# Kernel optimization log

Measured on AMD Instinct MI355X. Metric: run time of the kernel, lower is better.

Reference implementation:

```python
import jax, jax.numpy as jnp
import numpy as np
import math

N_HEAD = 12
N_EMBD = 768

def setup_inputs() -> dict:
    key = jax.random.key(0)
    ks = jax.random.split(key, 5)
    B, T, C = 4, 2048, N_EMBD
    s_attn = 1.0 / math.sqrt(C)
    return {
        "x": jax.random.normal(ks[0], (B, T, C), jnp.float32),
        "w_attn": jax.random.normal(ks[1], (C, 3 * C), jnp.float32) * s_attn,
        "b_attn": jnp.zeros((3 * C,), jnp.float32),
        "w_proj": jax.random.normal(ks[2], (C, C), jnp.float32) * s_attn,
        "b_proj": jnp.zeros((C,), jnp.float32),
    }

def reference(x, w_attn, b_attn, w_proj, b_proj):
    B, T, C = x.shape
    H = N_HEAD
    D = C // H
    qkv = x @ w_attn + b_attn  # [B,T,3C]
    q, k, v = jnp.split(qkv, 3, axis=-1)
    # [B,T,C] -> [B,H,T,D]
    q = q.reshape(B, T, H, D).transpose(0, 2, 1, 3)
    k = k.reshape(B, T, H, D).transpose(0, 2, 1, 3)
    v = v.reshape(B, T, H, D).transpose(0, 2, 1, 3)
    att = jnp.einsum('bhqd,bhkd->bhqk', q, k) * (1.0 / math.sqrt(D))
    causal = jnp.tril(jnp.ones((T, T), bool))
    att = jnp.where(causal[None, None], att, -jnp.inf)
    att = jax.nn.softmax(att, axis=-1)
    y = jnp.einsum('bhqk,bhkd->bhqd', att, v)  # [B,H,T,D]
    y = y.transpose(0, 2, 1, 3).reshape(B, T, C)
    return y @ w_proj + b_proj
```

## Files before the change

### kernel.cpp

```cpp
#include <hip/hip_runtime.h>
#include <hip/hip_bf16.h>

typedef unsigned short u16;
typedef __attribute__((ext_vector_type(4))) short bf16x4;
typedef __attribute__((ext_vector_type(8))) short bf16x8;
typedef __attribute__((ext_vector_type(16))) float f32x16;

#define NB_ 4
#define NT_ 2048
#define NC_ 768
#define NH_ 12
#define ND_ 64
#define NM_ (NB_*NT_)
#define KC_ 24

#define SCQ_ 0.18033688011112042f

__device__ __forceinline__ u16 f2bf(float f){
  union { float f; unsigned u; } c; c.f = f;
  unsigned u = c.u;
  return (u16)((u + 0x7fffu + ((u>>16)&1u)) >> 16);
}

__device__ __forceinline__ unsigned pkbf(float a, float b){
  __hip_bfloat162 h = __float22bfloat162_rn(make_float2(a,b));
  union { __hip_bfloat162 h; unsigned u; } c; c.h = h; return c.u;
}

__device__ __forceinline__ f32x16 mfma32(bf16x8 a, bf16x8 b, f32x16 c){
  return __builtin_amdgcn_mfma_f32_32x32x16_bf16(a, b, c, 0, 0, 0);
}

__device__ __forceinline__ void gload_lds16(const void* g, void* l){
  __builtin_amdgcn_global_load_lds(
    (const __attribute__((address_space(1))) void*)g,
    (__attribute__((address_space(3))) void*)l, 16, 0, 0);
}


__global__ __launch_bounds__(256) void prep_k(
    const float* __restrict__ x, const float* __restrict__ wa,
    const float* __restrict__ wp, u16* __restrict__ xb,
    u16* __restrict__ wat, u16* __restrict__ wpt){
  __shared__ float tile[32][33];
  const int bid = blockIdx.x, t = threadIdx.x;
  if (bid < 6144){
    int i = bid*256 + t;
    float4 v = ((const float4*)x)[i];
    int row = i / (NC_/4), k4 = (i % (NC_/4))*4;
    size_t off = (((size_t)(row>>7)*KC_ + (k4>>5))*4 + ((k4>>3)&3))*1024 + (row&127)*8 + (k4&7);
    bf16x4 o;
    o[0]=(short)f2bf(v.x); o[1]=(short)f2bf(v.y);
    o[2]=(short)f2bf(v.z); o[3]=(short)f2bf(v.w);
    *(bf16x4*)(xb + off) = o;
  } else {
    const float* in; u16* out; int c0, r0, Cc, PAN;
    if (bid < 6144 + 1728){
      int b = bid - 6144;
      in = wa; out = wat; Cc = 3*NC_; PAN = 96;
      c0 = (b % 72)*32; r0 = (b / 72)*32;
    } else {
      int b = bid - 7872;
      in = wp; out = wpt; Cc = NC_; PAN = 64;
      c0 = (b % 24)*32; r0 = (b / 24)*32;
    }
    int tx = t & 31, ty = t >> 5;
    #pragma unroll
    for (int j=0;j<32;j+=8) tile[ty+j][tx] = in[(size_t)(r0+ty+j)*Cc + c0+tx];
    __syncthreads();
    #pragma unroll
    for (int j=0;j<32;j+=8){
      int n = c0+ty+j, k = r0+tx;
      size_t off = ((size_t)(n/PAN)*KC_ + (k>>5))*(PAN*32)
                 + (size_t)((k>>3)&3)*(PAN*8) + (n%PAN)*8 + (k&7);
      out[off] = f2bf(tile[tx][ty+j]);
    }
  }
}

__global__ __launch_bounds__(256,3) void gemmQ(
  const u16* __restrict__ A, const u16* __restrict__ BT, const float* __restrict__ bias,
  u16* __restrict__ qo, u16* __restrict__ ko, u16* __restrict__ vo)
{
  __shared__ u16 lds[2][11264];
  const int t = threadIdx.x, w = t>>6, l = t&63;
  const int lq = l&31, h = l>>5;
  int sw = (blockIdx.x & 7)*96 + (blockIdx.x >> 3);
  const int rb = sw / 24, nb = sw % 24;
  const int brow = rb*256, bcol = nb*96;

  f32x16 acc[2][3];
  #pragma unroll
  for (int i=0;i<2;i++)
    #pragma unroll
    for (int j=0;j<3;j++)
      #pragma unroll
      for (int r=0;r<16;r++) acc[i][j][r] = 0.f;

  auto stage = [&](int buf, int kc){
    const u16* A0 = A  + ((size_t)((rb*2  )*KC_ + kc))*4096;
    const u16* A1 = A  + ((size_t)((rb*2+1)*KC_ + kc))*4096;
    const u16* Bg = BT + ((size_t)(nb*KC_ + kc))*3072;
    char* L = (char*)&lds[buf][0];
    gload_lds16(A0 + t*8,         L + t*16);
    gload_lds16(A0 + (256+t)*8,   L + (256+t)*16);
    gload_lds16(A1 + t*8,         L + 8192  + t*16);
    gload_lds16(A1 + (256+t)*8,   L + 8192  + (256+t)*16);
    gload_lds16(Bg + t*8,         L + 16384 + t*16);
    if (t < 128)
      gload_lds16(Bg + (256+t)*8, L + 16384 + (256+t)*16);
  };

  stage(0,0);
  int cur = 0;
  for (int kc=0; kc<KC_; ++kc){
    asm volatile("s_waitcnt vmcnt(0)\ns_barrier" ::: "memory");
    if (kc+1 < KC_) stage(cur^1, kc+1);
    const u16* La = &lds[cur][(w>>1)*4096];
    const u16* Lb = &lds[cur][8192];
    #pragma unroll
    for (int ks=0; ks<2; ++ks){
      bf16x8 af[2], bfr[3];
      #pragma unroll
      for (int mi=0;mi<2;mi++)
        af[mi]  = *(const bf16x8*)(La + ((2*ks+h)*128 + (w&1)*64 + mi*32 + lq)*8);
      #pragma unroll
      for (int nj=0;nj<3;nj++)
        bfr[nj] = *(const bf16x8*)(Lb + ((2*ks+h)*96 + nj*32 + lq)*8);
      __builtin_amdgcn_s_setprio(1);
      #pragma unroll
      for (int mi=0;mi<2;mi++)
        #pragma unroll
        for (int nj=0;nj<3;nj++)
          acc[mi][nj] = mfma32(af[mi], bfr[nj], acc[mi][nj]);
      __builtin_amdgcn_s_setprio(0);
    }
    cur ^= 1;
  }

  const int sec = nb >> 3;
  u16* outp = (sec==0) ? qo : (sec==1 ? ko : vo);
  #pragma unroll
  for (int nj=0;nj<3;nj++){
    int n = bcol + nj*32 + lq;
    int cc = n - sec*NC_;
    int hd = cc >> 6, d = cc & 63;
    float bs = bias[n];
    #pragma unroll
    for (int mi=0;mi<2;mi++)
      #pragma unroll
      for (int r=0;r<16;r++){
        int m = brow + w*64 + mi*32 + (r&3) + 8*(r>>2) + 4*h;
        int bb = m >> 11, tt = m & 2047;
        float v = acc[mi][nj][r] + bs;
        if (sec == 0) v *= SCQ_;
        size_t bhbase = ((size_t)bb*NH_ + hd)*((size_t)NT_*ND_);
        size_t off;
        if (sec == 0){
          off = bhbase + (size_t)tt*ND_ + d;
        } else if (sec == 1){
          off = bhbase + (size_t)(tt>>6)*4096 + (size_t)(d>>3)*512 + (tt&63)*8 + (d&7);
        } else {
          int p = (tt & ~15) | (h<<3) | (r&3) | (((r>>2)&1)<<2);
          off = bhbase + (size_t)(p>>6)*4096 + (size_t)((p&63)>>3)*512 + d*8 + (p&7);
        }
        outp[off] = f2bf(v);
      }
  }
}

__global__ __launch_bounds__(256,3) void gemmP(
  const u16* __restrict__ A, const u16* __restrict__ BT, const float* __restrict__ bias,
  float* __restrict__ fo)
{
  __shared__ u16 lds[2][6144];
  const int t = threadIdx.x, w = t>>6, l = t&63;
  const int lq = l&31, h = l>>5;
  int sw = (blockIdx.x & 7)*96 + (blockIdx.x >> 3);
  const int rb = sw / 12, nb = sw % 12;
  const int brow = rb*128, bcol = nb*64;
  const int wr = (w>>1)*64, wc = (w&1)*32;

  f32x16 acc[2];
  #pragma unroll
  for (int i=0;i<2;i++)
    #pragma unroll
    for (int r=0;r<16;r++) acc[i][r] = 0.f;

  auto stage = [&](int buf, int kc){
    const u16* Ag = A  + ((size_t)(rb*KC_ + kc))*4096;
    const u16* Bg = BT + ((size_t)(nb*KC_ + kc))*2048;
    char* La = (char*)&lds[buf][0];
    char* Lb = (char*)&lds[buf][4096];
    #pragma unroll
    for (int it=0; it<2; ++it)
      gload_lds16(Ag + (it*256+t)*8, La + (it*256+t)*16);
    gload_lds16(Bg + t*8, Lb + t*16);
  };

  stage(0,0);
  int cur = 0;
  for (int kc=0; kc<KC_; ++kc){
    asm volatile("s_waitcnt vmcnt(0)\ns_barrier" ::: "memory");
    if (kc+1 < KC_) stage(cur^1, kc+1);
    const u16* La = &lds[cur][0];
    const u16* Lb = &lds[cur][4096];
    #pragma unroll
    for (int ks=0; ks<2; ++ks){
      bf16x8 af[2], bfr;
      #pragma unroll
      for (int mi=0;mi<2;mi++)
        af[mi] = *(const bf16x8*)(La + ((2*ks+h)*128 + wr + mi*32 + lq)*8);
      bfr = *(const bf16x8*)(Lb + ((2*ks+h)*64 + wc + lq)*8);
      __builtin_amdgcn_s_setprio(1);
      #pragma unroll
      for (int mi=0;mi<2;mi++)
        acc[mi] = mfma32(af[mi], bfr, acc[mi]);
      __builtin_amdgcn_s_setprio(0);
    }
    cur ^= 1;
  }

  {
    int n = bcol + wc + lq;
    float bs = bias[n];
    #pragma unroll
    for (int mi=0;mi<2;mi++)
      #pragma unroll
      for (int r=0;r<16;r++){
        int m = brow + wr + mi*32 + (r&3) + 8*(r>>2) + 4*h;
        fo[(size_t)m*NC_ + n] = acc[mi][r] + bs;
      }
  }
}

__global__ __launch_bounds__(256,4) void attn_kernel(
    const u16* __restrict__ qg, const u16* __restrict__ kg,
    const u16* __restrict__ vg, u16* __restrict__ y)
{
  __shared__ u16 lds[2][8192];
  const int t = threadIdx.x, w = t>>6, l = t&63;
  const int lq = l&31, h = l>>5;
  const int bid = blockIdx.x;
  const int qt = 15 - (bid/48);
  const int bh = bid % 48;
  const int bb = bh / NH_, hh = bh % NH_;
  const u16* qp = qg + (size_t)bh*NT_*ND_;
  const u16* kp = kg + (size_t)bh*NT_*ND_;
  const u16* vp = vg + (size_t)bh*NT_*ND_;
  const int qmin = qt*128 + w*32;
  const int q = qmin + lq;

  bf16x8 Qf[4];
  {
    const u16* qr = qp + (size_t)q*ND_ + 8*h;
    #pragma unroll
    for (int ks=0; ks<4; ++ks) Qf[ks] = *(const bf16x8*)(qr + ks*16);
  }
  bf16x8 ones;
  #pragma unroll
  for (int i=0;i<8;i++) ones[i] = (short)0x3F80;

  f32x16 o0, o1, ls;
  #pragma unroll
  for (int r=0;r<16;r++){ o0[r]=0.f; o1[r]=0.f; ls[r]=0.f; }
  const int nc = 2*qt + 2;

  auto stage = [&](int buf, int c){
    const u16* kc2 = kp + c*4096;
    const u16* vc2 = vp + c*4096;
    #pragma unroll
    for (int it=0; it<2; ++it){
      gload_lds16(kc2 + (it*256 + t)*8, (char*)&lds[buf][0]    + (it*256 + t)*16);
      gload_lds16(vc2 + (it*256 + t)*8, (char*)&lds[buf][4096] + (it*256 + t)*16);
    }
  };

  stage(0,0);
  int cur = 0;
  for (int c=0; c<nc; ++c){
    asm volatile("s_waitcnt vmcnt(0)\ns_barrier" ::: "memory");
    if (c+1 < nc) stage(cur^1, c+1);

    const int kv0 = c*64;
    if (kv0 <= qmin + 31){
      const u16* Kb = &lds[cur][0];
      const u16* Vb = &lds[cur][4096];

      f32x16 s0, s1;
      #pragma unroll
      for (int r=0;r<16;r++){ s0[r]=0.f; s1[r]=0.f; }
      __builtin_amdgcn_s_setprio(1);
      #pragma unroll
      for (int ks=0; ks<4; ++ks){
        bf16x8 k0 = *(const bf16x8*)(Kb + ((2*ks+h)*64      + lq)*8);
        bf16x8 k1 = *(const bf16x8*)(Kb + ((2*ks+h)*64 + 32 + lq)*8);
        s0 = mfma32(k0, Qf[ks], s0);
        s1 = mfma32(k1, Qf[ks], s1);
      }
      __builtin_amdgcn_s_setprio(0);

      if (kv0 + 63 > qmin){
        #pragma unroll
        for (int r=0;r<16;r++){
          int kva = kv0 + (r&3) + 8*(r>>2) + 4*h;
          s0[r] = (kva      <= q) ? s0[r] : -3e38f;
          s1[r] = (kva + 32 <= q) ? s1[r] : -3e38f;
        }
      }

      union { unsigned wd[16]; bf16x8 v[4]; } pf;
      #pragma unroll
      for (int j=0;j<8;j++)
        pf.wd[j]   = pkbf(exp2f(s0[2*j]), exp2f(s0[2*j+1]));
      #pragma unroll
      for (int j=0;j<8;j++)
        pf.wd[8+j] = pkbf(exp2f(s1[2*j]), exp2f(s1[2*j+1]));

      __builtin_amdgcn_s_setprio(1);
      #pragma unroll
      for (int j=0;j<4;j++){
        bf16x8 v0 = *(const bf16x8*)(Vb + ((2*j+h)*64      + lq)*8);
        bf16x8 v1 = *(const bf16x8*)(Vb + ((2*j+h)*64 + 32 + lq)*8);
        o0 = mfma32(v0, pf.v[j], o0);
        o1 = mfma32(v1, pf.v[j], o1);
        ls = mfma32(ones, pf.v[j], ls);
      }
      __builtin_amdgcn_s_setprio(0);
    }
    cur ^= 1;
  }

  float inv = 1.f / ls[0];

  const int m = bb*NT_ + q;
  const int rbm = m>>7, rr = m&127;
  #pragma unroll
  for (int db=0; db<2; ++db){
    #pragma unroll
    for (int g2=0; g2<4; ++g2){
      float e0 = (db ? o1[g2*4+0] : o0[g2*4+0]) * inv;
      float e1 = (db ? o1[g2*4+1] : o0[g2*4+1]) * inv;
      float e2 = (db ? o1[g2*4+2] : o0[g2*4+2]) * inv;
      float e3 = (db ? o1[g2*4+3] : o0[g2*4+3]) * inv;
      unsigned w0 = pkbf(e0,e1), w1 = pkbf(e2,e3);
      int k = hh*ND_ + db*32 + g2*8 + 4*h;
      size_t off = (((size_t)rbm*KC_ + (k>>5))*4 + ((k>>3)&3))*1024 + rr*8 + (k&7);
      *(uint2*)(y + off) = make_uint2(w0, w1);
    }
  }
}

extern "C" void kernel_launch(void* const* d_in, const int* in_sizes, int n_in,
                              void* d_out, int out_size, void* d_ws, size_t ws_size,
                              hipStream_t stream) {
  const float* x  = (const float*)d_in[0];
  const float* wa = (const float*)d_in[1];
  const float* ba = (const float*)d_in[2];
  const float* wp = (const float*)d_in[3];
  const float* bp = (const float*)d_in[4];
  float* out = (float*)d_out;

  char* ws = (char*)d_ws;
  const size_t szXB = (size_t)NM_*NC_*2;
  const size_t szWA = (size_t)3*NC_*NC_*2;
  const size_t szWP = (size_t)NC_*NC_*2;
  const size_t szQ  = szXB;
  u16* xb  = (u16*)(ws);
  u16* wat = (u16*)(ws + szXB);
  u16* wpt = (u16*)(ws + szXB + szWA);
  u16* qb  = (u16*)(ws + szXB + szWA + szWP);
  u16* kb  = (u16*)((char*)qb + szQ);
  u16* vb  = (u16*)((char*)kb + szQ);
  u16* yb  = xb;

  prep_k<<<dim3(6144 + 1728 + 576), dim3(256), 0, stream>>>(x, wa, wp, xb, wat, wpt);
  gemmQ<<<dim3(768), dim3(256), 0, stream>>>(xb, wat, ba, qb, kb, vb);
  attn_kernel<<<dim3(NB_*NH_*(NT_/128)), dim3(256), 0, stream>>>(qb, kb, vb, yb);
  gemmP<<<dim3(768), dim3(256), 0, stream>>>(yb, wpt, bp, out);
}
```

Before: 128.4 us.

## Switch attention to 16x16x32 MFMA with 8 waves of 16 query rows

The attention kernel moves from 32x32x16 MFMA tiles with 4 waves of 32 query rows each to 16x16x32 MFMA tiles with 8 waves of 16 query rows each, launching 512 threads per block. The V layout written by the QKV GEMM epilogue is re-permuted to match the new P fragment layout. The aim is finer causal skipping per wave, fewer registers per wave and more waves per CU to hide latency. In exchange it issues more, smaller MFMAs and more LDS fragment reads per unit of work.

Result: no change. 125.8 us (median of 2 runs) (-2.0%).

```diff
diff --git a/kernel.cpp b/kernel.cpp
--- a/kernel.cpp
+++ b/kernel.cpp
@@ -4,6 +4,7 @@
 typedef unsigned short u16;
 typedef __attribute__((ext_vector_type(4))) short bf16x4;
 typedef __attribute__((ext_vector_type(8))) short bf16x8;
+typedef __attribute__((ext_vector_type(4))) float f32x4;
 typedef __attribute__((ext_vector_type(16))) float f32x16;
 
 #define NB_ 4
@@ -27,6 +28,9 @@
   union { __hip_bfloat162 h; unsigned u; } c; c.h = h; return c.u;
 }
 
+__device__ __forceinline__ f32x4 mfma16(bf16x8 a, bf16x8 b, f32x4 c){
+  return __builtin_amdgcn_mfma_f32_16x16x32_bf16(a, b, c, 0, 0, 0);
+}
 __device__ __forceinline__ f32x16 mfma32(bf16x8 a, bf16x8 b, f32x16 c){
   return __builtin_amdgcn_mfma_f32_32x32x16_bf16(a, b, c, 0, 0, 0);
 }
@@ -161,7 +165,8 @@
         } else if (sec == 1){
           off = bhbase + (size_t)(tt>>6)*4096 + (size_t)(d>>3)*512 + (tt&63)*8 + (d&7);
         } else {
-          int p = (tt & ~15) | (h<<3) | (r&3) | (((r>>2)&1)<<2);
+          int g2 = (2*(r>>2) + h) & 3;
+          int p = (tt & ~31) | (g2<<3) | (((r>>3)&1)<<2) | (r&3);
           off = bhbase + (size_t)(p>>6)*4096 + (size_t)((p&63)>>3)*512 + d*8 + (p&7);
         }
         outp[off] = f2bf(v);
@@ -234,13 +239,13 @@
   }
 }
 
-__global__ __launch_bounds__(256,4) void attn_kernel(
+__global__ __launch_bounds__(512,6) void attn_kernel(
     const u16* __restrict__ qg, const u16* __restrict__ kg,
     const u16* __restrict__ vg, u16* __restrict__ y)
 {
   __shared__ u16 lds[2][8192];
   const int t = threadIdx.x, w = t>>6, l = t&63;
-  const int lq = l&31, h = l>>5;
+  const int g = l>>4, lq16 = l&15;
   const int bid = blockIdx.x;
   const int qt = 15 - (bid/48);
   const int bh = bid % 48;
@@ -248,32 +253,33 @@
   const u16* qp = qg + (size_t)bh*NT_*ND_;
   const u16* kp = kg + (size_t)bh*NT_*ND_;
   const u16* vp = vg + (size_t)bh*NT_*ND_;
-  const int qmin = qt*128 + w*32;
-  const int q = qmin + lq;
-
-  bf16x8 Qf[4];
+  const int qw = qt*128 + w*16;
+  const int q = qw + lq16;
+
+  bf16x8 Qf[2];
   {
-    const u16* qr = qp + (size_t)q*ND_ + 8*h;
-    #pragma unroll
-    for (int ks=0; ks<4; ++ks) Qf[ks] = *(const bf16x8*)(qr + ks*16);
+    const u16* qr = qp + (size_t)q*ND_ + g*8;
+    Qf[0] = *(const bf16x8*)(qr);
+    Qf[1] = *(const bf16x8*)(qr + 32);
   }
   bf16x8 ones;
   #pragma unroll
   for (int i=0;i<8;i++) ones[i] = (short)0x3F80;
 
-  f32x16 o0, o1, ls;
-  #pragma unroll
-  for (int r=0;r<16;r++){ o0[r]=0.f; o1[r]=0.f; ls[r]=0.f; }
+  f32x4 acc[4], ls;
+  #pragma unroll
+  for (int i=0;i<4;i++)
+    #pragma unroll
+    for (int r=0;r<4;r++) acc[i][r] = 0.f;
+  #pragma unroll
+  for (int r=0;r<4;r++) ls[r] = 0.f;
   const int nc = 2*qt + 2;
 
   auto stage = [&](int buf, int c){
     const u16* kc2 = kp + c*4096;
     const u16* vc2 = vp + c*4096;
-    #pragma unroll
-    for (int it=0; it<2; ++it){
-      gload_lds16(kc2 + (it*256 + t)*8, (char*)&lds[buf][0]    + (it*256 + t)*16);
-      gload_lds16(vc2 + (it*256 + t)*8, (char*)&lds[buf][4096] + (it*256 + t)*16);
-    }
+    gload_lds16(kc2 + t*8, (char*)&lds[buf][0]    + t*16);
+    gload_lds16(vc2 + t*8, (char*)&lds[buf][4096] + t*16);
   };
 
   stage(0,0);
@@ -283,48 +289,53 @@
     if (c+1 < nc) stage(cur^1, c+1);
 
     const int kv0 = c*64;
-    if (kv0 <= qmin + 31){
+    if (kv0 <= qw + 15){
       const u16* Kb = &lds[cur][0];
       const u16* Vb = &lds[cur][4096];
 
-      f32x16 s0, s1;
-      #pragma unroll
-      for (int r=0;r<16;r++){ s0[r]=0.f; s1[r]=0.f; }
+      f32x4 s[4];
+      #pragma unroll
+      for (int t16=0;t16<4;t16++)
+        #pragma unroll
+        for (int r=0;r<4;r++) s[t16][r] = 0.f;
       __builtin_amdgcn_s_setprio(1);
       #pragma unroll
-      for (int ks=0; ks<4; ++ks){
-        bf16x8 k0 = *(const bf16x8*)(Kb + ((2*ks+h)*64      + lq)*8);
-        bf16x8 k1 = *(const bf16x8*)(Kb + ((2*ks+h)*64 + 32 + lq)*8);
-        s0 = mfma32(k0, Qf[ks], s0);
-        s1 = mfma32(k1, Qf[ks], s1);
-      }
+      for (int b=0;b<2;++b)
+        #pragma unroll
+        for (int t16=0;t16<4;++t16){
+          bf16x8 kf = *(const bf16x8*)(Kb + ((b*4+g)*64 + t16*16 + lq16)*8);
+          s[t16] = mfma16(kf, Qf[b], s[t16]);
+        }
       __builtin_amdgcn_s_setprio(0);
 
-      if (kv0 + 63 > qmin){
-        #pragma unroll
-        for (int r=0;r<16;r++){
-          int kva = kv0 + (r&3) + 8*(r>>2) + 4*h;
-          s0[r] = (kva      <= q) ? s0[r] : -3e38f;
-          s1[r] = (kva + 32 <= q) ? s1[r] : -3e38f;
+      if (kv0 + 63 > qw){
+        #pragma unroll
+        for (int t16=0;t16<4;++t16)
+          #pragma unroll
+          for (int r=0;r<4;++r){
+            int kva = kv0 + t16*16 + g*4 + r;
+            s[t16][r] = (kva <= q) ? s[t16][r] : -3e38f;
+          }
+      }
+
+      union { unsigned wd[4]; bf16x8 v; } pf[2];
+      #pragma unroll
+      for (int u=0;u<2;++u){
+        pf[u].wd[0] = pkbf(exp2f(s[2*u][0]),   exp2f(s[2*u][1]));
+        pf[u].wd[1] = pkbf(exp2f(s[2*u][2]),   exp2f(s[2*u][3]));
+        pf[u].wd[2] = pkbf(exp2f(s[2*u+1][0]), exp2f(s[2*u+1][1]));
+        pf[u].wd[3] = pkbf(exp2f(s[2*u+1][2]), exp2f(s[2*u+1][3]));
+      }
+
+      __builtin_amdgcn_s_setprio(1);
+      #pragma unroll
+      for (int u=0;u<2;++u){
+        #pragma unroll
+        for (int db=0;db<4;++db){
+          bf16x8 vf = *(const bf16x8*)(Vb + ((u*4+g)*64 + db*16 + lq16)*8);
+          acc[db] = mfma16(vf, pf[u].v, acc[db]);
         }
-      }
-
-      union { unsigned wd[16]; bf16x8 v[4]; } pf;
-      #pragma unroll
-      for (int j=0;j<8;j++)
-        pf.wd[j]   = pkbf(exp2f(s0[2*j]), exp2f(s0[2*j+1]));
-      #pragma unroll
-      for (int j=0;j<8;j++)
-        pf.wd[8+j] = pkbf(exp2f(s1[2*j]), exp2f(s1[2*j+1]));
-
-      __builtin_amdgcn_s_setprio(1);
-      #pragma unroll
-      for (int j=0;j<4;j++){
-        bf16x8 v0 = *(const bf16x8*)(Vb + ((2*j+h)*64      + lq)*8);
-        bf16x8 v1 = *(const bf16x8*)(Vb + ((2*j+h)*64 + 32 + lq)*8);
-        o0 = mfma32(v0, pf.v[j], o0);
-        o1 = mfma32(v1, pf.v[j], o1);
-        ls = mfma32(ones, pf.v[j], ls);
+        ls = mfma16(ones, pf[u].v, ls);
       }
       __builtin_amdgcn_s_setprio(0);
     }
@@ -336,18 +347,12 @@
   const int m = bb*NT_ + q;
   const int rbm = m>>7, rr = m&127;
   #pragma unroll
-  for (int db=0; db<2; ++db){
-    #pragma unroll
-    for (int g2=0; g2<4; ++g2){
-      float e0 = (db ? o1[g2*4+0] : o0[g2*4+0]) * inv;
-      float e1 = (db ? o1[g2*4+1] : o0[g2*4+1]) * inv;
-      float e2 = (db ? o1[g2*4+2] : o0[g2*4+2]) * inv;
-      float e3 = (db ? o1[g2*4+3] : o0[g2*4+3]) * inv;
-      unsigned w0 = pkbf(e0,e1), w1 = pkbf(e2,e3);
-      int k = hh*ND_ + db*32 + g2*8 + 4*h;
-      size_t off = (((size_t)rbm*KC_ + (k>>5))*4 + ((k>>3)&3))*1024 + rr*8 + (k&7);
-      *(uint2*)(y + off) = make_uint2(w0, w1);
-    }
+  for (int db=0; db<4; ++db){
+    unsigned w0 = pkbf(acc[db][0]*inv, acc[db][1]*inv);
+    unsigned w1 = pkbf(acc[db][2]*inv, acc[db][3]*inv);
+    int k = hh*ND_ + db*16 + g*4;
+    size_t off = (((size_t)rbm*KC_ + (k>>5))*4 + ((k>>3)&3))*1024 + rr*8 + (k&7);
+    *(uint2*)(y + off) = make_uint2(w0, w1);
   }
 }
 
@@ -376,6 +381,6 @@
 
   prep_k<<<dim3(6144 + 1728 + 576), dim3(256), 0, stream>>>(x, wa, wp, xb, wat, wpt);
   gemmQ<<<dim3(768), dim3(256), 0, stream>>>(xb, wat, ba, qb, kb, vb);
-  attn_kernel<<<dim3(NB_*NH_*(NT_/128)), dim3(256), 0, stream>>>(qb, kb, vb, yb);
+  attn_kernel<<<dim3(NB_*NH_*(NT_/128)), dim3(512), 0, stream>>>(qb, kb, vb, yb);
   gemmP<<<dim3(768), dim3(256), 0, stream>>>(yb, wpt, bp, out);
 }
```
